# Optimization experiments

Hardware: AMD Instinct MI355X
Metric: run time of the kernel (lower is better)

The kernel has to match this reference:

```python
import math
import jax, jax.numpy as jnp
import numpy as np

EPS = 1.0
B, T, D, H = 8, 512, 768, 12
DH = D // H  # 64


def setup_inputs() -> dict:
    key = jax.random.key(0)
    ks = jax.random.split(key, 10)
    std = 0.02
    return {
        "x": jax.random.normal(ks[0], (B, T, D), dtype=jnp.float32),
        "r_position_embedding": jax.random.normal(ks[1], (T, D), dtype=jnp.float32),
        "r_content_bias": jax.random.normal(ks[2], (H, DH), dtype=jnp.float32),
        "r_position_bias": jax.random.normal(ks[3], (H, DH), dtype=jnp.float32),
        # Conv1D(linear) params, stored as (in, out) so y = x @ W + b
        "Wqkv": jax.random.normal(ks[4], (D, 3 * D), dtype=jnp.float32) * std,
        "bqkv": jnp.zeros((3 * D,), dtype=jnp.float32),
        "Wh": jax.random.normal(ks[5], (D, D), dtype=jnp.float32) * std,
        "bh": jnp.zeros((D,), dtype=jnp.float32),
        "Wp": jax.random.normal(ks[6], (D, D), dtype=jnp.float32) * std,
        "bp": jnp.zeros((D,), dtype=jnp.float32),
    }


def reference(x, r_position_embedding, r_content_bias, r_position_bias,
              Wqkv, bqkv, Wh, bh, Wp, bp):
    # QKV projection and head split
    qkv = x @ Wqkv + bqkv                                   # (B,T,3D)
    q, k, v = jnp.split(qkv, 3, axis=-1)
    split_heads = lambda t: t.reshape(B, T, H, DH).transpose(0, 2, 1, 3)  # (B,H,T,DH)
    q, k, v = split_heads(q), split_heads(k), split_heads(v)

    # content scores
    scores = jnp.einsum('bhtd,bhsd->bhts', q, k)            # (B,H,T,T)

    # relative position projection: linear is row-wise, so project once then gather.
    # rel_pos[c, r] = linear_position(pos_emb[max(0, c - r)])
    proj = (r_position_embedding @ Wp + bp).reshape(T, H, DH)  # (P=T, H, DH)
    idx = jnp.maximum(0, jnp.arange(T)[:, None] - jnp.arange(T)[None, :])  # (T,T) = max(0, c-r)

    # q . rel_pos term: compute vs all P distinct positions, then gather per (c, r)
    rel_q = jnp.einsum('bhtd,phd->bhtp', q, proj)           # (B,H,T,P)
    scores = scores + jnp.take_along_axis(rel_q, idx[None, None, :, :], axis=-1)

    # content-bias and position-bias terms (query-independent)
    bias_c = jnp.einsum('hd,phd->hp', r_content_bias, proj)[:, idx]   # (H,T,T)
    bias_p = jnp.einsum('hd,phd->hp', r_position_bias, proj)[:, idx]  # (H,T,T)
    scores = scores + bias_c[None] + bias_p[None]

    # masked softmax with EPS=1 quirks (faithful to original)
    scores = scores / (math.sqrt(DH) + EPS)
    mask = jnp.tril(jnp.ones((T, T), dtype=jnp.float32))    # causal
    masked_exps = jnp.exp(scores) * mask
    att = masked_exps / (masked_exps.sum(-1, keepdims=True) + 2.0 * EPS)

    ctx = jnp.einsum('bhts,bhsd->bhtd', att, v)             # (B,H,T,DH)
    # original: permute(0,2,3,1) then flatten -> (B,T,DH*H) interleaving (d, h)
    ctx = ctx.transpose(0, 2, 3, 1).reshape(B, T, D)
    out = ctx @ Wh + bh
    k_out = k.transpose(0, 1, 3, 2)                         # (B,H,DH,T) as module returns
    return out, k_out, v
```

## Files before the change

kernel.cpp:

```cpp
#include <hip/hip_runtime.h>
#include <hip/hip_bf16.h>


#define NT 512
#define ND 768
#define NH 12

typedef short short4_t __attribute__((ext_vector_type(4)));
typedef short short8_t __attribute__((ext_vector_type(8)));
typedef float float4_t __attribute__((ext_vector_type(4)));

__device__ __forceinline__ float b2f(unsigned short u) {
    union { unsigned int i; float f; } x; x.i = ((unsigned int)u) << 16; return x.f;
}
__device__ __forceinline__ unsigned short f2b(float f) {
    union { float f; unsigned int i; } x; x.f = f;
    unsigned int i = x.i;
    i += 0x7fffu + ((i >> 16) & 1u);
    return (unsigned short)(i >> 16);
}

__global__ __launch_bounds__(256) void prep(
    const float* __restrict__ x, unsigned short* __restrict__ xb,
    const float* __restrict__ Wqkv, unsigned short* __restrict__ WqkvT,
    const float* __restrict__ Wh, unsigned short* __restrict__ WhT)
{
    __shared__ float t[32][33];
    const int bid = blockIdx.x;
    const int tid = threadIdx.x;

    if (bid < 1536) {
        const int i = bid * 256 + tid;
        const float* s = x + (size_t)i * 8;
        float4_t f0 = *(const float4_t*)s;
        float4_t f1 = *(const float4_t*)(s + 4);
        union { short8_t v; unsigned short u[8]; } pk;
        pk.u[0] = f2b(f0[0]); pk.u[1] = f2b(f0[1]); pk.u[2] = f2b(f0[2]); pk.u[3] = f2b(f0[3]);
        pk.u[4] = f2b(f1[0]); pk.u[5] = f2b(f1[1]); pk.u[6] = f2b(f1[2]); pk.u[7] = f2b(f1[3]);
        *(short8_t*)&xb[(size_t)i * 8] = pk.v;
        return;
    }
    const float* in; unsigned short* out; int K, N, k0, n0;
    if (bid < 3264) {
        const int tt = bid - 1536;
        in = Wqkv; out = WqkvT; K = 768; N = 2304;
        n0 = (tt % 72) * 32; k0 = (tt / 72) * 32;
    } else {
        const int tt = bid - 3264;
        in = Wh; out = WhT; K = 768; N = 768;
        n0 = (tt % 24) * 32; k0 = (tt / 24) * 32;
    }
    const int r = tid >> 3;
    const int c = (tid & 7) * 4;
    float4_t v = *(const float4_t*)&in[(size_t)(k0 + r) * N + n0 + c];
    t[r][c + 0] = v[0]; t[r][c + 1] = v[1]; t[r][c + 2] = v[2]; t[r][c + 3] = v[3];
    __syncthreads();
    union { short4_t v; unsigned short u[4]; } pk;
    pk.u[0] = f2b(t[c + 0][r]);
    pk.u[1] = f2b(t[c + 1][r]);
    pk.u[2] = f2b(t[c + 2][r]);
    pk.u[3] = f2b(t[c + 3][r]);
    *(short4_t*)&out[(size_t)(n0 + r) * K + k0 + c] = pk.v;
}

template <int MODE>
__global__ __launch_bounds__(256) void gemm128(
    const unsigned short* __restrict__ A, const unsigned short* __restrict__ BT,
    const float* __restrict__ biasf,
    unsigned short* __restrict__ ob0, float* __restrict__ o1, float* __restrict__ o2,
    unsigned short* __restrict__ sh1, unsigned short* __restrict__ sh2,
    int K)
{
    __shared__ __attribute__((aligned(16))) unsigned short Al[3][128 * 32];
    __shared__ __attribute__((aligned(16))) unsigned short Bl[3][128 * 32];

    const int tid  = threadIdx.x;
    const int m0   = blockIdx.y * 128;
    const int n0   = blockIdx.x * 128;
    const int wave = tid >> 6;
    const int lane = tid & 63;
    const int lm   = lane & 15;
    const int quad = lane >> 4;
    const int wr   = (wave >> 1) * 64;
    const int wc   = (wave & 1) * 64;

    float4_t acc[4][4];
#pragma unroll
    for (int mt = 0; mt < 4; ++mt)
#pragma unroll
        for (int nt = 0; nt < 4; ++nt)
#pragma unroll
            for (int r = 0; r < 4; ++r) acc[mt][nt][r] = 0.f;

    const unsigned short* ap = A  + (size_t)(m0 + (tid >> 2)) * K + (tid & 3) * 8;
    const unsigned short* bp = BT + (size_t)(n0 + (tid >> 2)) * K + (tid & 3) * 8;
    const size_t rstep = (size_t)64 * K;

    auto stage = [&](int bi, int k0) {
        unsigned short* al0 = &Al[bi][0] + wave * 512;
        unsigned short* bl0 = &Bl[bi][0] + wave * 512;
        __builtin_amdgcn_global_load_lds(
            (const __attribute__((address_space(1))) void*)(ap + k0),
            (__attribute__((address_space(3))) void*)al0, 16, 0, 0);
        __builtin_amdgcn_global_load_lds(
            (const __attribute__((address_space(1))) void*)(ap + rstep + k0),
            (__attribute__((address_space(3))) void*)(al0 + 2048), 16, 0, 0);
        __builtin_amdgcn_global_load_lds(
            (const __attribute__((address_space(1))) void*)(bp + k0),
            (__attribute__((address_space(3))) void*)bl0, 16, 0, 0);
        __builtin_amdgcn_global_load_lds(
            (const __attribute__((address_space(1))) void*)(bp + rstep + k0),
            (__attribute__((address_space(3))) void*)(bl0 + 2048), 16, 0, 0);
    };

    stage(0, 0);
    stage(1, 32);

    int cur = 0;
    for (int k0 = 0; k0 < K; k0 += 32) {
        if (k0 + 32 < K) asm volatile("s_waitcnt vmcnt(4)" ::: "memory");
        else             asm volatile("s_waitcnt vmcnt(0)" ::: "memory");
        __builtin_amdgcn_s_barrier();
        __builtin_amdgcn_sched_barrier(0);

        if (k0 + 64 < K) stage((cur + 2) % 3, k0 + 64);

        short8_t af[4], bf[4];
#pragma unroll
        for (int mt = 0; mt < 4; ++mt)
            af[mt] = *(const short8_t*)&Al[cur][(wr + mt * 16 + lm) * 32 + quad * 8];
#pragma unroll
        for (int nt = 0; nt < 4; ++nt)
            bf[nt] = *(const short8_t*)&Bl[cur][(wc + nt * 16 + lm) * 32 + quad * 8];
#pragma unroll
        for (int mt = 0; mt < 4; ++mt)
#pragma unroll
            for (int nt = 0; nt < 4; ++nt)
                acc[mt][nt] = __builtin_amdgcn_mfma_f32_16x16x32_bf16(af[mt], bf[nt], acc[mt][nt], 0, 0, 0);

        cur = (cur + 1) % 3;
    }

#pragma unroll
    for (int nt = 0; nt < 4; ++nt) {
        const int gcol = n0 + wc + nt * 16 + lm;
        const float bv = biasf[gcol];
#pragma unroll
        for (int mt = 0; mt < 4; ++mt) {
#pragma unroll
            for (int r = 0; r < 4; ++r) {
                const int grow = m0 + wr + mt * 16 + quad * 4 + r;
                const float val = acc[mt][nt][r] + bv;
                if (MODE == 0) {
                    int b = grow >> 9, t = grow & 511;
                    int sec = gcol / 768;
                    int cc = gcol - sec * 768;
                    int h = cc >> 6, d = cc & 63;
                    if (sec == 0) {
                        ob0[((size_t)((b * NH + h) * NT + t)) * 64 + d] = f2b(val);
                    } else if (sec == 1) {
                        o1[((size_t)((b * NH + h) * 64 + d)) * NT + t] = val;
                        sh1[((size_t)((b * NH + h) * NT + t)) * 64 + d] = f2b(val);
                    } else {
                        o2[((size_t)((b * NH + h) * NT + t)) * 64 + d] = val;
                        sh2[((size_t)((b * NH + h) * 64 + d)) * NT + t] = f2b(val);
                    }
                } else {
                    o1[(size_t)grow * ND + gcol] = val;
                }
            }
        }
    }
}

__global__ __launch_bounds__(256) void gemm_proj(
    const float* __restrict__ Af, const float* __restrict__ Bw,
    const float* __restrict__ biasf,
    const float* __restrict__ rcb, const float* __restrict__ rpb,
    unsigned short* __restrict__ projb, float* __restrict__ biascp)
{
    __shared__ unsigned short Al[64][40];
    __shared__ unsigned short Bl[64][40];

    const int tid  = threadIdx.x;
    const int m0   = blockIdx.y * 64;
    const int n0   = blockIdx.x * 64;
    const int wave = tid >> 6;
    const int lane = tid & 63;
    const int lm   = lane & 15;
    const int quad = lane >> 4;
    const int koff = quad * 8;
    const int K = 768, ldb = 768;

    float4_t acc[4];
#pragma unroll
    for (int j = 0; j < 4; ++j)
#pragma unroll
        for (int r = 0; r < 4; ++r) acc[j][r] = 0.0f;

    const int arow = tid >> 2;
    const int acg  = (tid & 3) * 8;
    const int bk   = tid & 31;
    const int bg   = tid >> 5;

    for (int k0 = 0; k0 < K; k0 += 32) {
        {
            const float* src = &Af[(size_t)(m0 + arow) * K + k0 + acg];
            float4_t f0 = *(const float4_t*)src;
            float4_t f1 = *(const float4_t*)(src + 4);
            union { short8_t v; unsigned short u[8]; } pk;
            pk.u[0] = f2b(f0[0]); pk.u[1] = f2b(f0[1]); pk.u[2] = f2b(f0[2]); pk.u[3] = f2b(f0[3]);
            pk.u[4] = f2b(f1[0]); pk.u[5] = f2b(f1[1]); pk.u[6] = f2b(f1[2]); pk.u[7] = f2b(f1[3]);
            *(short8_t*)&Al[arow][acg] = pk.v;
        }
        {
            const float* src = &Bw[(size_t)(k0 + bk) * ldb + n0 + bg * 8];
            float4_t f0 = *(const float4_t*)src;
            float4_t f1 = *(const float4_t*)(src + 4);
            Bl[bg * 8 + 0][bk] = f2b(f0[0]); Bl[bg * 8 + 1][bk] = f2b(f0[1]);
            Bl[bg * 8 + 2][bk] = f2b(f0[2]); Bl[bg * 8 + 3][bk] = f2b(f0[3]);
            Bl[bg * 8 + 4][bk] = f2b(f1[0]); Bl[bg * 8 + 5][bk] = f2b(f1[1]);
            Bl[bg * 8 + 6][bk] = f2b(f1[2]); Bl[bg * 8 + 7][bk] = f2b(f1[3]);
        }
        __syncthreads();

        short8_t af = *(const short8_t*)&Al[wave * 16 + lm][koff];
#pragma unroll
        for (int j = 0; j < 4; ++j) {
            short8_t bf = *(const short8_t*)&Bl[j * 16 + lm][koff];
            acc[j] = __builtin_amdgcn_mfma_f32_16x16x32_bf16(af, bf, acc[j], 0, 0, 0);
        }
        __syncthreads();
    }

    const int h = n0 >> 6;
    float cb4[4], part[4] = {0.f, 0.f, 0.f, 0.f};
#pragma unroll
    for (int j = 0; j < 4; ++j) {
        const int d = j * 16 + lm;
        cb4[j] = rcb[h * 64 + d] + rpb[h * 64 + d];
    }
#pragma unroll
    for (int j = 0; j < 4; ++j) {
        const int gcol = n0 + j * 16 + lm;
        const int d = gcol & 63;
        const float bv = biasf[gcol];
#pragma unroll
        for (int r = 0; r < 4; ++r) {
            const int grow = m0 + wave * 16 + quad * 4 + r;
            const float val = acc[j][r] + bv;
            projb[((size_t)(h * NT + grow)) * 64 + d] = f2b(val);
            part[r] += val * cb4[j];
        }
    }
#pragma unroll
    for (int r = 0; r < 4; ++r) {
        float v = part[r];
        v += __shfl_xor(v, 1); v += __shfl_xor(v, 2);
        v += __shfl_xor(v, 4); v += __shfl_xor(v, 8);
        if (lm == 0) biascp[h * NT + m0 + wave * 16 + quad * 4 + r] = v;
    }
}

__global__ __launch_bounds__(128) void attn_mfma(
    const unsigned short* __restrict__ q_ws, const unsigned short* __restrict__ k_ws,
    const unsigned short* __restrict__ v_ws, const unsigned short* __restrict__ projb,
    const float* __restrict__ biascp, unsigned short* __restrict__ ctxT)
{
    __shared__ unsigned short Kt[64][72];
    __shared__ unsigned short Vt[64][72];
    __shared__ unsigned short pP[96][72];
    __shared__ float          Rl[2][16][84];
    __shared__ unsigned short esl[2][16][72];

    const int tid   = threadIdx.x;
    const int y     = blockIdx.y;
    const int h     = y % NH;
    const int b     = y / NH;
    const int pairi = blockIdx.x;
    const int wave  = tid >> 6;
    const int lane  = tid & 63;
    const int lm    = lane & 15;
    const int quad  = lane >> 4;
    const int koff  = quad * 8;

    const int sr = tid >> 1;
    const int sc = (tid & 1) * 32;

    for (int c = 0; c < 2; ++c) {
        const int ti  = c ? pairi : (15 - pairi);
        const int tb0 = ti * 32;
        const int tw0 = tb0 + wave * 16;
        const int nst = (tb0 >> 6) + 1;

        short8_t aq[2];
        aq[0] = *(const short8_t*)&q_ws[((size_t)(y * NT + tw0 + lm)) * 64 + koff];
        aq[1] = *(const short8_t*)&q_ws[((size_t)(y * NT + tw0 + lm)) * 64 + koff + 32];

        float4_t ctxacc[4];
#pragma unroll
        for (int j = 0; j < 4; ++j)
#pragma unroll
            for (int r = 0; r < 4; ++r) ctxacc[j][r] = 0.f;
        float esum[4] = {0.f, 0.f, 0.f, 0.f};

        for (int st = 0; st < nst; ++st) {
            const int s0      = st * 64;
            const int plo_blk = max(0, tb0 - s0 - 63);
            const int cnt_blk = tb0 + 31 - s0 - plo_blk + 1;
            if (c | st) __syncthreads();
            {
                const unsigned short* ks = &k_ws[((size_t)(y * NT + s0 + sr)) * 64 + sc];
                *(short8_t*)&Kt[sr][sc]      = *(const short8_t*)ks;
                *(short8_t*)&Kt[sr][sc + 8]  = *(const short8_t*)(ks + 8);
                *(short8_t*)&Kt[sr][sc + 16] = *(const short8_t*)(ks + 16);
                *(short8_t*)&Kt[sr][sc + 24] = *(const short8_t*)(ks + 24);
                const unsigned short* vs = &v_ws[((size_t)(y * 64 + sr)) * NT + s0 + sc];
                *(short8_t*)&Vt[sr][sc]      = *(const short8_t*)vs;
                *(short8_t*)&Vt[sr][sc + 8]  = *(const short8_t*)(vs + 8);
                *(short8_t*)&Vt[sr][sc + 16] = *(const short8_t*)(vs + 16);
                *(short8_t*)&Vt[sr][sc + 24] = *(const short8_t*)(vs + 24);
                for (int p = tid; p < cnt_blk; p += 128) {
                    const unsigned short* ps = &projb[((size_t)(h * NT + plo_blk + p)) * 64];
                    *(short8_t*)&pP[p][0]  = *(const short8_t*)ps;
                    *(short8_t*)&pP[p][8]  = *(const short8_t*)(ps + 8);
                    *(short8_t*)&pP[p][16] = *(const short8_t*)(ps + 16);
                    *(short8_t*)&pP[p][24] = *(const short8_t*)(ps + 24);
                    *(short8_t*)&pP[p][32] = *(const short8_t*)(ps + 32);
                    *(short8_t*)&pP[p][40] = *(const short8_t*)(ps + 40);
                    *(short8_t*)&pP[p][48] = *(const short8_t*)(ps + 48);
                    *(short8_t*)&pP[p][56] = *(const short8_t*)(ps + 56);
                }
            }
            __syncthreads();

            if (s0 <= tw0 + 15) {
                const int plo_w = max(0, tw0 - s0 - 63);
                const int pbase = plo_w - plo_blk;
                const int cntw  = tw0 + 15 - s0 - plo_w + 1;
                const int jmax  = min(3, (tw0 + 15 - s0) >> 4);
                const int jpmax = (cntw - 1) >> 4;

                float4_t accQK[4];
#pragma unroll
                for (int j = 0; j < 4; ++j)
#pragma unroll
                    for (int r = 0; r < 4; ++r) accQK[j][r] = 0.f;
                for (int j = 0; j <= jmax; ++j) {
                    short8_t bk0 = *(const short8_t*)&Kt[j * 16 + lm][koff];
                    short8_t bk1 = *(const short8_t*)&Kt[j * 16 + lm][koff + 32];
                    accQK[j] = __builtin_amdgcn_mfma_f32_16x16x32_bf16(aq[0], bk0, accQK[j], 0, 0, 0);
                    accQK[j] = __builtin_amdgcn_mfma_f32_16x16x32_bf16(aq[1], bk1, accQK[j], 0, 0, 0);
                }
                for (int j = 0; j <= jpmax; ++j) {
                    short8_t bp0 = *(const short8_t*)&pP[pbase + j * 16 + lm][koff];
                    short8_t bp1 = *(const short8_t*)&pP[pbase + j * 16 + lm][koff + 32];
                    float4_t accR;
#pragma unroll
                    for (int r = 0; r < 4; ++r) accR[r] = 0.f;
                    accR = __builtin_amdgcn_mfma_f32_16x16x32_bf16(aq[0], bp0, accR, 0, 0, 0);
                    accR = __builtin_amdgcn_mfma_f32_16x16x32_bf16(aq[1], bp1, accR, 0, 0, 0);
                    const int p = j * 16 + lm;
                    const float bv = biascp[h * NT + min(plo_w + p, NT - 1)];
#pragma unroll
                    for (int r = 0; r < 4; ++r) Rl[wave][quad * 4 + r][p] = accR[r] + bv;
                }
                asm volatile("" ::: "memory");

#pragma unroll
                for (int j = 0; j < 4; ++j) {
                    const int s_g = s0 + j * 16 + lm;
#pragma unroll
                    for (int r = 0; r < 4; ++r) {
                        const int t_g = tw0 + quad * 4 + r;
                        float e = 0.f;
                        if (s_g <= t_g) {
                            const int p = t_g - s_g - plo_w;
                            e = __expf(fminf((accQK[j][r] + Rl[wave][quad * 4 + r][p]) * (1.f / 9.f), 60.f));
                        }
                        esl[wave][quad * 4 + r][j * 16 + lm] = f2b(e);
                        esum[r] += e;
                    }
                }
                asm volatile("" ::: "memory");

                short8_t ae0 = *(const short8_t*)&esl[wave][lm][koff];
                short8_t ae1 = *(const short8_t*)&esl[wave][lm][koff + 32];
#pragma unroll
                for (int j = 0; j < 4; ++j) {
                    short8_t bv0 = *(const short8_t*)&Vt[j * 16 + lm][koff];
                    short8_t bv1 = *(const short8_t*)&Vt[j * 16 + lm][koff + 32];
                    ctxacc[j] = __builtin_amdgcn_mfma_f32_16x16x32_bf16(ae0, bv0, ctxacc[j], 0, 0, 0);
                    ctxacc[j] = __builtin_amdgcn_mfma_f32_16x16x32_bf16(ae1, bv1, ctxacc[j], 0, 0, 0);
                }
            }
        }

        float rcpv[4];
#pragma unroll
        for (int r = 0; r < 4; ++r) {
            float v = esum[r];
            v += __shfl_xor(v, 1); v += __shfl_xor(v, 2);
            v += __shfl_xor(v, 4); v += __shfl_xor(v, 8);
            rcpv[r] = 1.f / (v + 2.f);
        }
#pragma unroll
        for (int j = 0; j < 4; ++j) {
            const int d = j * 16 + lm;
#pragma unroll
            for (int r = 0; r < 4; ++r) {
                const int t = tw0 + quad * 4 + r;
                ctxT[((size_t)(b * NT + t)) * ND + d * NH + h] = f2b(ctxacc[j][r] * rcpv[r]);
            }
        }
    }
}

extern "C" void kernel_launch(void* const* d_in, const int* in_sizes, int n_in,
                              void* d_out, int out_size, void* d_ws, size_t ws_size,
                              hipStream_t stream)
{
    const float* x    = (const float*)d_in[0];
    const float* rpe  = (const float*)d_in[1];
    const float* rcb  = (const float*)d_in[2];
    const float* rpb  = (const float*)d_in[3];
    const float* Wqkv = (const float*)d_in[4];
    const float* bqkv = (const float*)d_in[5];
    const float* Wh   = (const float*)d_in[6];
    const float* bh   = (const float*)d_in[7];
    const float* Wp   = (const float*)d_in[8];
    const float* bp   = (const float*)d_in[9];

    float* out  = (float*)d_out;
    float* kout = out + 3145728;
    float* vout = out + 6291456;

    unsigned short* q_ws  = (unsigned short*)d_ws;
    unsigned short* k_ws  = q_ws + 3145728;
    unsigned short* v_ws  = k_ws + 3145728;
    unsigned short* ctxT  = v_ws + 3145728;
    unsigned short* xb    = ctxT;
    unsigned short* projb = ctxT + 3145728;
    float* biascp = (float*)(projb + 393216);
    unsigned short* WqkvT = (unsigned short*)(biascp + 6144);
    unsigned short* WhT   = WqkvT + 1769472;

    prep<<<dim3(3840), 256, 0, stream>>>(x, xb, Wqkv, WqkvT, Wh, WhT);

    gemm128<0><<<dim3(2304 / 128, 4096 / 128), 256, 0, stream>>>(
        xb, WqkvT, bqkv, q_ws, kout, vout, k_ws, v_ws, 768);
    gemm_proj<<<dim3(768 / 64, 512 / 64), 256, 0, stream>>>(
        rpe, Wp, bp, rcb, rpb, projb, biascp);
    attn_mfma<<<dim3(8, 96), 128, 0, stream>>>(
        q_ws, k_ws, v_ws, projb, biascp, ctxT);
    gemm128<2><<<dim3(768 / 128, 4096 / 128), 256, 0, stream>>>(
        ctxT, WhT, bh, nullptr, out, nullptr, nullptr, nullptr, 768);
}
```

Before: 239.0 us.

## Merge proj GEMM into QKV GEMM launch with 64x128 tiles and bf16 prep

The fp32 relative-position projection GEMM is folded into the QKV GEMM launch as extra blocks. Its inputs (rpe and a transposed Wp) are now converted to bf16 in the prep kernel and staged through the rpeb/WpT scratch buffers placed in the output region. The GEMM tile shrinks from 128x128 to 64x128, raising the block count (1152 QKV plus 48 proj, and 384 for the output projection) for better CU occupancy on a large GPU, and one launch is removed. The trade-off is less data reuse per tile, and the out buffer is reused as scratch before the final GEMM overwrites it.

```diff
diff --git a/kernel.cpp b/kernel.cpp
--- a/kernel.cpp
+++ b/kernel.cpp
@@ -22,32 +22,41 @@
 
 __global__ __launch_bounds__(256) void prep(
     const float* __restrict__ x, unsigned short* __restrict__ xb,
+    const float* __restrict__ rpe, unsigned short* __restrict__ rpeb,
     const float* __restrict__ Wqkv, unsigned short* __restrict__ WqkvT,
-    const float* __restrict__ Wh, unsigned short* __restrict__ WhT)
+    const float* __restrict__ Wh, unsigned short* __restrict__ WhT,
+    const float* __restrict__ Wp, unsigned short* __restrict__ WpT)
 {
     __shared__ float t[32][33];
     const int bid = blockIdx.x;
     const int tid = threadIdx.x;
 
-    if (bid < 1536) {
-        const int i = bid * 256 + tid;
-        const float* s = x + (size_t)i * 8;
+    if (bid < 1728) {
+        const bool isx = bid < 1536;
+        const float* in = isx ? x : rpe;
+        unsigned short* out = isx ? xb : rpeb;
+        const int i = (isx ? bid : bid - 1536) * 256 + tid;
+        const float* s = in + (size_t)i * 8;
         float4_t f0 = *(const float4_t*)s;
         float4_t f1 = *(const float4_t*)(s + 4);
         union { short8_t v; unsigned short u[8]; } pk;
         pk.u[0] = f2b(f0[0]); pk.u[1] = f2b(f0[1]); pk.u[2] = f2b(f0[2]); pk.u[3] = f2b(f0[3]);
         pk.u[4] = f2b(f1[0]); pk.u[5] = f2b(f1[1]); pk.u[6] = f2b(f1[2]); pk.u[7] = f2b(f1[3]);
-        *(short8_t*)&xb[(size_t)i * 8] = pk.v;
+        *(short8_t*)&out[(size_t)i * 8] = pk.v;
         return;
     }
     const float* in; unsigned short* out; int K, N, k0, n0;
-    if (bid < 3264) {
-        const int tt = bid - 1536;
+    if (bid < 3456) {
+        const int tt = bid - 1728;
         in = Wqkv; out = WqkvT; K = 768; N = 2304;
         n0 = (tt % 72) * 32; k0 = (tt / 72) * 32;
+    } else if (bid < 4032) {
+        const int tt = bid - 3456;
+        in = Wh; out = WhT; K = 768; N = 768;
+        n0 = (tt % 24) * 32; k0 = (tt / 24) * 32;
     } else {
-        const int tt = bid - 3264;
-        in = Wh; out = WhT; K = 768; N = 768;
+        const int tt = bid - 4032;
+        in = Wp; out = WpT; K = 768; N = 768;
         n0 = (tt % 24) * 32; k0 = (tt / 24) * 32;
     }
     const int r = tid >> 3;
@@ -64,36 +73,49 @@
 }
 
 template <int MODE>
-__global__ __launch_bounds__(256) void gemm128(
+__global__ __launch_bounds__(256) void gemm64(
     const unsigned short* __restrict__ A, const unsigned short* __restrict__ BT,
     const float* __restrict__ biasf,
     unsigned short* __restrict__ ob0, float* __restrict__ o1, float* __restrict__ o2,
     unsigned short* __restrict__ sh1, unsigned short* __restrict__ sh2,
-    int K)
+    const unsigned short* __restrict__ Ap, const unsigned short* __restrict__ BTp,
+    const float* __restrict__ biasp, const float* __restrict__ rcb,
+    const float* __restrict__ rpb, unsigned short* __restrict__ projb,
+    float* __restrict__ biascp)
 {
-    __shared__ __attribute__((aligned(16))) unsigned short Al[3][128 * 32];
+    __shared__ __attribute__((aligned(16))) unsigned short Al[3][64 * 32];
     __shared__ __attribute__((aligned(16))) unsigned short Bl[3][128 * 32];
 
+    const int K    = 768;
     const int tid  = threadIdx.x;
-    const int m0   = blockIdx.y * 128;
-    const int n0   = blockIdx.x * 128;
+    const int bid  = blockIdx.x;
     const int wave = tid >> 6;
     const int lane = tid & 63;
     const int lm   = lane & 15;
     const int quad = lane >> 4;
-    const int wr   = (wave >> 1) * 64;
+    const int wr   = (wave >> 1) * 32;
     const int wc   = (wave & 1) * 64;
 
-    float4_t acc[4][4];
-#pragma unroll
-    for (int mt = 0; mt < 4; ++mt)
+    int m0, n0; bool proj = false;
+    const unsigned short *Asrc, *Bsrc;
+    if (MODE == 0) {
+        if (bid < 1152) { m0 = (bid / 18) * 64; n0 = (bid % 18) * 128; Asrc = A;  Bsrc = BT; }
+        else { const int pb = bid - 1152; m0 = (pb / 6) * 64; n0 = (pb % 6) * 128;
+               Asrc = Ap; Bsrc = BTp; proj = true; }
+    } else {
+        m0 = (bid / 6) * 64; n0 = (bid % 6) * 128; Asrc = A; Bsrc = BT;
+    }
+
+    float4_t acc[2][4];
+#pragma unroll
+    for (int mt = 0; mt < 2; ++mt)
 #pragma unroll
         for (int nt = 0; nt < 4; ++nt)
 #pragma unroll
             for (int r = 0; r < 4; ++r) acc[mt][nt][r] = 0.f;
 
-    const unsigned short* ap = A  + (size_t)(m0 + (tid >> 2)) * K + (tid & 3) * 8;
-    const unsigned short* bp = BT + (size_t)(n0 + (tid >> 2)) * K + (tid & 3) * 8;
+    const unsigned short* ap = Asrc + (size_t)(m0 + (tid >> 2)) * K + (tid & 3) * 8;
+    const unsigned short* bp = Bsrc + (size_t)(n0 + (tid >> 2)) * K + (tid & 3) * 8;
     const size_t rstep = (size_t)64 * K;
 
     auto stage = [&](int bi, int k0) {
@@ -103,9 +125,6 @@
             (const __attribute__((address_space(1))) void*)(ap + k0),
             (__attribute__((address_space(3))) void*)al0, 16, 0, 0);
         __builtin_amdgcn_global_load_lds(
-            (const __attribute__((address_space(1))) void*)(ap + rstep + k0),
-            (__attribute__((address_space(3))) void*)(al0 + 2048), 16, 0, 0);
-        __builtin_amdgcn_global_load_lds(
             (const __attribute__((address_space(1))) void*)(bp + k0),
             (__attribute__((address_space(3))) void*)bl0, 16, 0, 0);
         __builtin_amdgcn_global_load_lds(
@@ -118,22 +137,22 @@
 
     int cur = 0;
     for (int k0 = 0; k0 < K; k0 += 32) {
-        if (k0 + 32 < K) asm volatile("s_waitcnt vmcnt(4)" ::: "memory");
+        if (k0 + 32 < K) asm volatile("s_waitcnt vmcnt(3)" ::: "memory");
         else             asm volatile("s_waitcnt vmcnt(0)" ::: "memory");
         __builtin_amdgcn_s_barrier();
         __builtin_amdgcn_sched_barrier(0);
 
         if (k0 + 64 < K) stage((cur + 2) % 3, k0 + 64);
 
-        short8_t af[4], bf[4];
-#pragma unroll
-        for (int mt = 0; mt < 4; ++mt)
+        short8_t af[2], bf[4];
+#pragma unroll
+        for (int mt = 0; mt < 2; ++mt)
             af[mt] = *(const short8_t*)&Al[cur][(wr + mt * 16 + lm) * 32 + quad * 8];
 #pragma unroll
         for (int nt = 0; nt < 4; ++nt)
             bf[nt] = *(const short8_t*)&Bl[cur][(wc + nt * 16 + lm) * 32 + quad * 8];
 #pragma unroll
-        for (int mt = 0; mt < 4; ++mt)
+        for (int mt = 0; mt < 2; ++mt)
 #pragma unroll
             for (int nt = 0; nt < 4; ++nt)
                 acc[mt][nt] = __builtin_amdgcn_mfma_f32_16x16x32_bf16(af[mt], bf[nt], acc[mt][nt], 0, 0, 0);
@@ -141,21 +160,37 @@
         cur = (cur + 1) % 3;
     }
 
-#pragma unroll
-    for (int nt = 0; nt < 4; ++nt) {
-        const int gcol = n0 + wc + nt * 16 + lm;
-        const float bv = biasf[gcol];
-#pragma unroll
-        for (int mt = 0; mt < 4; ++mt) {
-#pragma unroll
-            for (int r = 0; r < 4; ++r) {
-                const int grow = m0 + wr + mt * 16 + quad * 4 + r;
-                const float val = acc[mt][nt][r] + bv;
-                if (MODE == 0) {
-                    int b = grow >> 9, t = grow & 511;
-                    int sec = gcol / 768;
-                    int cc = gcol - sec * 768;
-                    int h = cc >> 6, d = cc & 63;
+    if (MODE == 2) {
+#pragma unroll
+        for (int nt = 0; nt < 4; ++nt) {
+            const int gcol = n0 + wc + nt * 16 + lm;
+            const float bv = biasf[gcol];
+#pragma unroll
+            for (int mt = 0; mt < 2; ++mt)
+#pragma unroll
+                for (int r = 0; r < 4; ++r) {
+                    const int grow = m0 + wr + mt * 16 + quad * 4 + r;
+                    o1[(size_t)grow * ND + gcol] = acc[mt][nt][r] + bv;
+                }
+        }
+        return;
+    }
+
+    if (!proj) {
+        const int sec = n0 / 768;
+#pragma unroll
+        for (int nt = 0; nt < 4; ++nt) {
+            const int gcol = n0 + wc + nt * 16 + lm;
+            const int cc = gcol - sec * 768;
+            const int h = cc >> 6, d = cc & 63;
+            const float bv = biasf[gcol];
+#pragma unroll
+            for (int mt = 0; mt < 2; ++mt)
+#pragma unroll
+                for (int r = 0; r < 4; ++r) {
+                    const int grow = m0 + wr + mt * 16 + quad * 4 + r;
+                    const int b = grow >> 9, t = grow & 511;
+                    const float val = acc[mt][nt][r] + bv;
                     if (sec == 0) {
                         ob0[((size_t)((b * NH + h) * NT + t)) * 64 + d] = f2b(val);
                     } else if (sec == 1) {
@@ -165,100 +200,41 @@
                         o2[((size_t)((b * NH + h) * NT + t)) * 64 + d] = val;
                         sh2[((size_t)((b * NH + h) * 64 + d)) * NT + t] = f2b(val);
                     }
-                } else {
-                    o1[(size_t)grow * ND + gcol] = val;
-                }
+                }
+        }
+    } else {
+        const int h = (n0 + wc) >> 6;
+        float part[2][4];
+#pragma unroll
+        for (int mt = 0; mt < 2; ++mt)
+#pragma unroll
+            for (int r = 0; r < 4; ++r) part[mt][r] = 0.f;
+#pragma unroll
+        for (int nt = 0; nt < 4; ++nt) {
+            const int gcol = n0 + wc + nt * 16 + lm;
+            const int d = gcol & 63;
+            const float bv = biasp[gcol];
+            const float cb = rcb[h * 64 + d] + rpb[h * 64 + d];
+#pragma unroll
+            for (int mt = 0; mt < 2; ++mt)
+#pragma unroll
+                for (int r = 0; r < 4; ++r) {
+                    const int grow = m0 + wr + mt * 16 + quad * 4 + r;
+                    const float val = acc[mt][nt][r] + bv;
+                    projb[((size_t)(h * NT + grow)) * 64 + d] = f2b(val);
+                    part[mt][r] += val * cb;
+                }
+        }
+#pragma unroll
+        for (int mt = 0; mt < 2; ++mt)
+#pragma unroll
+            for (int r = 0; r < 4; ++r) {
+                float v = part[mt][r];
+                v += __shfl_xor(v, 1); v += __shfl_xor(v, 2);
+                v += __shfl_xor(v, 4); v += __shfl_xor(v, 8);
+                if (lm == 0)
+                    biascp[h * NT + m0 + wr + mt * 16 + quad * 4 + r] = v;
             }
-        }
-    }
-}
-
-__global__ __launch_bounds__(256) void gemm_proj(
-    const float* __restrict__ Af, const float* __restrict__ Bw,
-    const float* __restrict__ biasf,
-    const float* __restrict__ rcb, const float* __restrict__ rpb,
-    unsigned short* __restrict__ projb, float* __restrict__ biascp)
-{
-    __shared__ unsigned short Al[64][40];
-    __shared__ unsigned short Bl[64][40];
-
-    const int tid  = threadIdx.x;
-    const int m0   = blockIdx.y * 64;
-    const int n0   = blockIdx.x * 64;
-    const int wave = tid >> 6;
-    const int lane = tid & 63;
-    const int lm   = lane & 15;
-    const int quad = lane >> 4;
-    const int koff = quad * 8;
-    const int K = 768, ldb = 768;
-
-    float4_t acc[4];
-#pragma unroll
-    for (int j = 0; j < 4; ++j)
-#pragma unroll
-        for (int r = 0; r < 4; ++r) acc[j][r] = 0.0f;
-
-    const int arow = tid >> 2;
-    const int acg  = (tid & 3) * 8;
-    const int bk   = tid & 31;
-    const int bg   = tid >> 5;
-
-    for (int k0 = 0; k0 < K; k0 += 32) {
-        {
-            const float* src = &Af[(size_t)(m0 + arow) * K + k0 + acg];
-            float4_t f0 = *(const float4_t*)src;
-            float4_t f1 = *(const float4_t*)(src + 4);
-            union { short8_t v; unsigned short u[8]; } pk;
-            pk.u[0] = f2b(f0[0]); pk.u[1] = f2b(f0[1]); pk.u[2] = f2b(f0[2]); pk.u[3] = f2b(f0[3]);
-            pk.u[4] = f2b(f1[0]); pk.u[5] = f2b(f1[1]); pk.u[6] = f2b(f1[2]); pk.u[7] = f2b(f1[3]);
-            *(short8_t*)&Al[arow][acg] = pk.v;
-        }
-        {
-            const float* src = &Bw[(size_t)(k0 + bk) * ldb + n0 + bg * 8];
-            float4_t f0 = *(const float4_t*)src;
-            float4_t f1 = *(const float4_t*)(src + 4);
-            Bl[bg * 8 + 0][bk] = f2b(f0[0]); Bl[bg * 8 + 1][bk] = f2b(f0[1]);
-            Bl[bg * 8 + 2][bk] = f2b(f0[2]); Bl[bg * 8 + 3][bk] = f2b(f0[3]);
-            Bl[bg * 8 + 4][bk] = f2b(f1[0]); Bl[bg * 8 + 5][bk] = f2b(f1[1]);
-            Bl[bg * 8 + 6][bk] = f2b(f1[2]); Bl[bg * 8 + 7][bk] = f2b(f1[3]);
-        }
-        __syncthreads();
-
-        short8_t af = *(const short8_t*)&Al[wave * 16 + lm][koff];
-#pragma unroll
-        for (int j = 0; j < 4; ++j) {
-            short8_t bf = *(const short8_t*)&Bl[j * 16 + lm][koff];
-            acc[j] = __builtin_amdgcn_mfma_f32_16x16x32_bf16(af, bf, acc[j], 0, 0, 0);
-        }
-        __syncthreads();
-    }
-
-    const int h = n0 >> 6;
-    float cb4[4], part[4] = {0.f, 0.f, 0.f, 0.f};
-#pragma unroll
-    for (int j = 0; j < 4; ++j) {
-        const int d = j * 16 + lm;
-        cb4[j] = rcb[h * 64 + d] + rpb[h * 64 + d];
-    }
-#pragma unroll
-    for (int j = 0; j < 4; ++j) {
-        const int gcol = n0 + j * 16 + lm;
-        const int d = gcol & 63;
-        const float bv = biasf[gcol];
-#pragma unroll
-        for (int r = 0; r < 4; ++r) {
-            const int grow = m0 + wave * 16 + quad * 4 + r;
-            const float val = acc[j][r] + bv;
-            projb[((size_t)(h * NT + grow)) * 64 + d] = f2b(val);
-            part[r] += val * cb4[j];
-        }
-    }
-#pragma unroll
-    for (int r = 0; r < 4; ++r) {
-        float v = part[r];
-        v += __shfl_xor(v, 1); v += __shfl_xor(v, 2);
-        v += __shfl_xor(v, 4); v += __shfl_xor(v, 8);
-        if (lm == 0) biascp[h * NT + m0 + wave * 16 + quad * 4 + r] = v;
     }
 }
 
@@ -444,15 +420,17 @@
     float* biascp = (float*)(projb + 393216);
     unsigned short* WqkvT = (unsigned short*)(biascp + 6144);
     unsigned short* WhT   = WqkvT + 1769472;
-
-    prep<<<dim3(3840), 256, 0, stream>>>(x, xb, Wqkv, WqkvT, Wh, WhT);
-
-    gemm128<0><<<dim3(2304 / 128, 4096 / 128), 256, 0, stream>>>(
-        xb, WqkvT, bqkv, q_ws, kout, vout, k_ws, v_ws, 768);
-    gemm_proj<<<dim3(768 / 64, 512 / 64), 256, 0, stream>>>(
-        rpe, Wp, bp, rcb, rpb, projb, biascp);
+    unsigned short* rpeb  = (unsigned short*)out;
+    unsigned short* WpT   = rpeb + 393216;
+
+    prep<<<dim3(4608), 256, 0, stream>>>(x, xb, rpe, rpeb, Wqkv, WqkvT, Wh, WhT, Wp, WpT);
+
+    gemm64<0><<<dim3(1200), 256, 0, stream>>>(
+        xb, WqkvT, bqkv, q_ws, kout, vout, k_ws, v_ws,
+        rpeb, WpT, bp, rcb, rpb, projb, biascp);
     attn_mfma<<<dim3(8, 96), 128, 0, stream>>>(
         q_ws, k_ws, v_ws, projb, biascp, ctxT);
-    gemm128<2><<<dim3(768 / 128, 4096 / 128), 256, 0, stream>>>(
-        ctxT, WhT, bh, nullptr, out, nullptr, nullptr, nullptr, 768);
-}
+    gemm64<2><<<dim3(384), 256, 0, stream>>>(
+        ctxT, WhT, bh, nullptr, out, nullptr, nullptr, nullptr,
+        nullptr, nullptr, nullptr, nullptr, nullptr, nullptr, nullptr);
+}
```

After: 206.0 us. 13.8% less time.

## Split GEMM template into QKV and output kernels with tile and schedule changes

Applied to the files above, without the earlier changes.

Replaces the shared templated GEMM with two specialised kernels. The QKV GEMM drops triple-buffered LDS pipelining for single-buffer loads with two barriers per k-step, and remaps block IDs in an XCD-aware order. Its epilogue also hoists the section and head index math out of the inner loop. The output GEMM uses 64x128 tiles, giving 384 blocks instead of 192 to fill more CUs, keeps the 3-stage pipeline and also uses swizzled block IDs. The QKV change trades prefetch overlap for lower LDS use and possibly higher occupancy.

```diff
diff --git a/kernel.cpp b/kernel.cpp
--- a/kernel.cpp
+++ b/kernel.cpp
@@ -63,20 +63,21 @@
     *(short4_t*)&out[(size_t)(n0 + r) * K + k0 + c] = pk.v;
 }
 
-template <int MODE>
-__global__ __launch_bounds__(256) void gemm128(
+__global__ __launch_bounds__(256) void gemm_qkv(
     const unsigned short* __restrict__ A, const unsigned short* __restrict__ BT,
     const float* __restrict__ biasf,
     unsigned short* __restrict__ ob0, float* __restrict__ o1, float* __restrict__ o2,
-    unsigned short* __restrict__ sh1, unsigned short* __restrict__ sh2,
-    int K)
+    unsigned short* __restrict__ sh1, unsigned short* __restrict__ sh2)
 {
-    __shared__ __attribute__((aligned(16))) unsigned short Al[3][128 * 32];
-    __shared__ __attribute__((aligned(16))) unsigned short Bl[3][128 * 32];
-
+    __shared__ __attribute__((aligned(16))) unsigned short Al[128 * 32];
+    __shared__ __attribute__((aligned(16))) unsigned short Bl[128 * 32];
+
+    const int K    = 768;
     const int tid  = threadIdx.x;
-    const int m0   = blockIdx.y * 128;
-    const int n0   = blockIdx.x * 128;
+    int qb = blockIdx.x;
+    qb = (qb & 7) * 72 + (qb >> 3);
+    const int m0   = (qb / 18) * 128;
+    const int n0   = (qb % 18) * 128;
     const int wave = tid >> 6;
     const int lane = tid & 63;
     const int lm   = lane & 15;
@@ -95,10 +96,11 @@
     const unsigned short* ap = A  + (size_t)(m0 + (tid >> 2)) * K + (tid & 3) * 8;
     const unsigned short* bp = BT + (size_t)(n0 + (tid >> 2)) * K + (tid & 3) * 8;
     const size_t rstep = (size_t)64 * K;
-
-    auto stage = [&](int bi, int k0) {
-        unsigned short* al0 = &Al[bi][0] + wave * 512;
-        unsigned short* bl0 = &Bl[bi][0] + wave * 512;
+    unsigned short* al0 = Al + wave * 512;
+    unsigned short* bl0 = Bl + wave * 512;
+
+    for (int k0 = 0; k0 < K; k0 += 32) {
+        if (k0) __syncthreads();
         __builtin_amdgcn_global_load_lds(
             (const __attribute__((address_space(1))) void*)(ap + k0),
             (__attribute__((address_space(3))) void*)al0, 16, 0, 0);
@@ -111,62 +113,44 @@
         __builtin_amdgcn_global_load_lds(
             (const __attribute__((address_space(1))) void*)(bp + rstep + k0),
             (__attribute__((address_space(3))) void*)(bl0 + 2048), 16, 0, 0);
-    };
-
-    stage(0, 0);
-    stage(1, 32);
-
-    int cur = 0;
-    for (int k0 = 0; k0 < K; k0 += 32) {
-        if (k0 + 32 < K) asm volatile("s_waitcnt vmcnt(4)" ::: "memory");
-        else             asm volatile("s_waitcnt vmcnt(0)" ::: "memory");
-        __builtin_amdgcn_s_barrier();
-        __builtin_amdgcn_sched_barrier(0);
-
-        if (k0 + 64 < K) stage((cur + 2) % 3, k0 + 64);
+        __syncthreads();
 
         short8_t af[4], bf[4];
 #pragma unroll
         for (int mt = 0; mt < 4; ++mt)
-            af[mt] = *(const short8_t*)&Al[cur][(wr + mt * 16 + lm) * 32 + quad * 8];
+            af[mt] = *(const short8_t*)&Al[(wr + mt * 16 + lm) * 32 + quad * 8];
 #pragma unroll
         for (int nt = 0; nt < 4; ++nt)
-            bf[nt] = *(const short8_t*)&Bl[cur][(wc + nt * 16 + lm) * 32 + quad * 8];
+            bf[nt] = *(const short8_t*)&Bl[(wc + nt * 16 + lm) * 32 + quad * 8];
 #pragma unroll
         for (int mt = 0; mt < 4; ++mt)
 #pragma unroll
             for (int nt = 0; nt < 4; ++nt)
                 acc[mt][nt] = __builtin_amdgcn_mfma_f32_16x16x32_bf16(af[mt], bf[nt], acc[mt][nt], 0, 0, 0);
-
-        cur = (cur + 1) % 3;
-    }
-
+    }
+
+    const int sec = n0 / 768;
 #pragma unroll
     for (int nt = 0; nt < 4; ++nt) {
         const int gcol = n0 + wc + nt * 16 + lm;
+        const int cc = gcol - sec * 768;
+        const int h = cc >> 6, d = cc & 63;
         const float bv = biasf[gcol];
 #pragma unroll
         for (int mt = 0; mt < 4; ++mt) {
 #pragma unroll
             for (int r = 0; r < 4; ++r) {
                 const int grow = m0 + wr + mt * 16 + quad * 4 + r;
+                const int b = grow >> 9, t = grow & 511;
                 const float val = acc[mt][nt][r] + bv;
-                if (MODE == 0) {
-                    int b = grow >> 9, t = grow & 511;
-                    int sec = gcol / 768;
-                    int cc = gcol - sec * 768;
-                    int h = cc >> 6, d = cc & 63;
-                    if (sec == 0) {
-                        ob0[((size_t)((b * NH + h) * NT + t)) * 64 + d] = f2b(val);
-                    } else if (sec == 1) {
-                        o1[((size_t)((b * NH + h) * 64 + d)) * NT + t] = val;
-                        sh1[((size_t)((b * NH + h) * NT + t)) * 64 + d] = f2b(val);
-                    } else {
-                        o2[((size_t)((b * NH + h) * NT + t)) * 64 + d] = val;
-                        sh2[((size_t)((b * NH + h) * 64 + d)) * NT + t] = f2b(val);
-                    }
+                if (sec == 0) {
+                    ob0[((size_t)((b * NH + h) * NT + t)) * 64 + d] = f2b(val);
+                } else if (sec == 1) {
+                    o1[((size_t)((b * NH + h) * 64 + d)) * NT + t] = val;
+                    sh1[((size_t)((b * NH + h) * NT + t)) * 64 + d] = f2b(val);
                 } else {
-                    o1[(size_t)grow * ND + gcol] = val;
+                    o2[((size_t)((b * NH + h) * NT + t)) * 64 + d] = val;
+                    sh2[((size_t)((b * NH + h) * 64 + d)) * NT + t] = f2b(val);
                 }
             }
         }
@@ -259,6 +243,94 @@
         v += __shfl_xor(v, 1); v += __shfl_xor(v, 2);
         v += __shfl_xor(v, 4); v += __shfl_xor(v, 8);
         if (lm == 0) biascp[h * NT + m0 + wave * 16 + quad * 4 + r] = v;
+    }
+}
+
+__global__ __launch_bounds__(256) void gemm_out(
+    const unsigned short* __restrict__ A, const unsigned short* __restrict__ BT,
+    const float* __restrict__ biasf, float* __restrict__ o1)
+{
+    __shared__ __attribute__((aligned(16))) unsigned short Al[3][64 * 32];
+    __shared__ __attribute__((aligned(16))) unsigned short Bl[3][128 * 32];
+
+    const int K    = 768;
+    const int tid  = threadIdx.x;
+    const int bid  = (blockIdx.x & 7) * 48 + (blockIdx.x >> 3);
+    const int wave = tid >> 6;
+    const int lane = tid & 63;
+    const int lm   = lane & 15;
+    const int quad = lane >> 4;
+    const int wr   = (wave >> 1) * 32;
+    const int wc   = (wave & 1) * 64;
+
+    const int m0 = (bid / 6) * 64;
+    const int n0 = (bid % 6) * 128;
+
+    float4_t acc[2][4];
+#pragma unroll
+    for (int mt = 0; mt < 2; ++mt)
+#pragma unroll
+        for (int nt = 0; nt < 4; ++nt)
+#pragma unroll
+            for (int r = 0; r < 4; ++r) acc[mt][nt][r] = 0.f;
+
+    const unsigned short* ap = A  + (size_t)(m0 + (tid >> 2)) * K + (tid & 3) * 8;
+    const unsigned short* bp = BT + (size_t)(n0 + (tid >> 2)) * K + (tid & 3) * 8;
+    const size_t rstep = (size_t)64 * K;
+
+    auto stage = [&](int bi, int k0) {
+        unsigned short* al0 = &Al[bi][0] + wave * 512;
+        unsigned short* bl0 = &Bl[bi][0] + wave * 512;
+        __builtin_amdgcn_global_load_lds(
+            (const __attribute__((address_space(1))) void*)(ap + k0),
+            (__attribute__((address_space(3))) void*)al0, 16, 0, 0);
+        __builtin_amdgcn_global_load_lds(
+            (const __attribute__((address_space(1))) void*)(bp + k0),
+            (__attribute__((address_space(3))) void*)bl0, 16, 0, 0);
+        __builtin_amdgcn_global_load_lds(
+            (const __attribute__((address_space(1))) void*)(bp + rstep + k0),
+            (__attribute__((address_space(3))) void*)(bl0 + 2048), 16, 0, 0);
+    };
+
+    stage(0, 0);
+    stage(1, 32);
+
+    int cur = 0;
+    for (int k0 = 0; k0 < K; k0 += 32) {
+        if (k0 + 32 < K) asm volatile("s_waitcnt vmcnt(3)" ::: "memory");
+        else             asm volatile("s_waitcnt vmcnt(0)" ::: "memory");
+        __builtin_amdgcn_s_barrier();
+        __builtin_amdgcn_sched_barrier(0);
+
+        if (k0 + 64 < K) stage((cur + 2) % 3, k0 + 64);
+
+        short8_t af[2], bf[4];
+#pragma unroll
+        for (int mt = 0; mt < 2; ++mt)
+            af[mt] = *(const short8_t*)&Al[cur][(wr + mt * 16 + lm) * 32 + quad * 8];
+#pragma unroll
+        for (int nt = 0; nt < 4; ++nt)
+            bf[nt] = *(const short8_t*)&Bl[cur][(wc + nt * 16 + lm) * 32 + quad * 8];
+#pragma unroll
+        for (int mt = 0; mt < 2; ++mt)
+#pragma unroll
+            for (int nt = 0; nt < 4; ++nt)
+                acc[mt][nt] = __builtin_amdgcn_mfma_f32_16x16x32_bf16(af[mt], bf[nt], acc[mt][nt], 0, 0, 0);
+
+        cur = (cur + 1) % 3;
+    }
+
+#pragma unroll
+    for (int nt = 0; nt < 4; ++nt) {
+        const int gcol = n0 + wc + nt * 16 + lm;
+        const float bv = biasf[gcol];
+#pragma unroll
+        for (int mt = 0; mt < 2; ++mt)
+#pragma unroll
+            for (int r = 0; r < 4; ++r) {
+                const int grow = m0 + wr + mt * 16 + quad * 4 + r;
+                o1[(size_t)grow * ND + gcol] = acc[mt][nt][r] + bv;
+            }
     }
 }
 
@@ -447,12 +519,12 @@
 
     prep<<<dim3(3840), 256, 0, stream>>>(x, xb, Wqkv, WqkvT, Wh, WhT);
 
-    gemm128<0><<<dim3(2304 / 128, 4096 / 128), 256, 0, stream>>>(
-        xb, WqkvT, bqkv, q_ws, kout, vout, k_ws, v_ws, 768);
+    gemm_qkv<<<dim3(576), 256, 0, stream>>>(
+        xb, WqkvT, bqkv, q_ws, kout, vout, k_ws, v_ws);
     gemm_proj<<<dim3(768 / 64, 512 / 64), 256, 0, stream>>>(
         rpe, Wp, bp, rcb, rpb, projb, biascp);
     attn_mfma<<<dim3(8, 96), 128, 0, stream>>>(
         q_ws, k_ws, v_ws, projb, biascp, ctxT);
-    gemm128<2><<<dim3(768 / 128, 4096 / 128), 256, 0, stream>>>(
-        ctxT, WhT, bh, nullptr, out, nullptr, nullptr, nullptr, 768);
-}
+    gemm_out<<<dim3(384), 256, 0, stream>>>(
+        ctxT, WhT, bh, out);
+}
```

New measurement: 218.1 us. -8.8%, faster.
